# Kernel optimization log

Measured on AMD Instinct MI355X. Metric: run time of the kernel, lower is better.

The kernel has to match this reference:

```python
import jax, jax.numpy as jnp
import numpy as np

N, C, B, CTX = 1_000_000, 64, 8, 256
EPS = 1e-5


def setup_inputs() -> dict:
    key = jax.random.key(0)
    k1, k2, k3, k4, k5, k6 = jax.random.split(key, 6)
    x = jax.random.normal(k1, (N, C), dtype=jnp.float32)
    dataset_token = jax.random.normal(k2, (B, CTX), dtype=jnp.float32)
    # coors[:, 0] holds the (sorted) batch index per point; other cols are voxel coords
    batch_idx = jnp.sort(jax.random.randint(k3, (N,), 0, B))
    other = jax.random.randint(k4, (N, 3), 0, 1024)
    coors = jnp.concatenate([batch_idx[:, None], other], axis=1).astype(jnp.int64)
    # LayerNorm (base_norm) params
    gamma = jnp.ones((C,), dtype=jnp.float32)
    beta = jnp.zeros((C,), dtype=jnp.float32)
    # MLP: SiLU -> Linear(CTX, 2C)
    W = jax.random.normal(k5, (2 * C, CTX), dtype=jnp.float32) * (1.0 / np.sqrt(CTX))
    b = jax.random.normal(k6, (2 * C,), dtype=jnp.float32) * 0.02
    return {"x": x, "dataset_token": dataset_token, "gamma": gamma, "beta": beta,
            "W": W, "b": b, "coors": coors}


def reference(x, dataset_token, gamma, beta, W, b, coors):
    # base_norm = LayerNorm over features
    mu = jnp.mean(x, axis=-1, keepdims=True)
    var = jnp.mean(jnp.square(x - mu), axis=-1, keepdims=True)
    out = (x - mu) * jax.lax.rsqrt(var + EPS) * gamma + beta  # (N, C)
    # FiLM conditioning: mlp(dataset_token) -> (shift, scale) per batch element
    h = jnp.dot(jax.nn.silu(dataset_token), W.T) + b  # (B, 2C)
    shift, scale = jnp.split(h, 2, axis=1)            # each (B, C)
    idx = coors[:, 0]                                  # (N,) batch id per point
    # fused gather + affine over all N points (replaces the python loop)
    return out * (1.0 + scale[idx]) + shift[idx]
```

## Files before the change

kernel.cpp:

```cpp
#include <hip/hip_runtime.h>
#include <math.h>

#define EPS 1e-5f
#define NROWS 1000000
#define C 64
#define B 8
#define CTX 256

__global__ __launch_bounds__(1024) void token_gemm(
        const float* __restrict__ dt, const float* __restrict__ W,
        const float* __restrict__ bias, float* __restrict__ ws) {
    __shared__ float sdt[B * CTX];
    int t = threadIdx.x;
    for (int i = t; i < B * CTX; i += 1024) {
        float v = dt[i];
        sdt[i] = v / (1.0f + expf(-v));
    }
    __syncthreads();

    int j = t >> 7;
    int k = t & 127;
    const float* __restrict__ wrow = W + k * CTX;
    const float* __restrict__ drow = sdt + j * CTX;
    float acc = 0.0f;
    #pragma unroll 8
    for (int i = 0; i < CTX; ++i) acc += wrow[i] * drow[i];
    acc += bias[k];

    if (k < C) ws[j * C + k] = acc;
    else       ws[512 + j * C + (k - C)] = 1.0f + acc;
}

__global__ __launch_bounds__(256) void ln_mod(
        const float* __restrict__ x, const float* __restrict__ gamma,
        const float* __restrict__ beta, const int* __restrict__ coors,
        const float* __restrict__ h, float* __restrict__ out, int n) {
    __shared__ float sh[1024];
    int t = threadIdx.x;
    ((float4*)sh)[t] = ((const float4*)h)[t];
    __syncthreads();

    int group = t >> 4;
    int lane  = t & 15;
    int row = blockIdx.x * 16 + group;
    if (row >= n) return;

    float4 v = ((const float4*)x)[row * 16 + lane];

    float s  = v.x + v.y + v.z + v.w;
    float ss = v.x * v.x + v.y * v.y + v.z * v.z + v.w * v.w;
    #pragma unroll
    for (int m = 1; m < 16; m <<= 1) {
        s  += __shfl_xor(s,  m, 16);
        ss += __shfl_xor(ss, m, 16);
    }
    float mu   = s * (1.0f / 64.0f);
    float var  = ss * (1.0f / 64.0f) - mu * mu;
    float rstd = rsqrtf(var + EPS);

    int bidx = coors[row * 4];

    float4 g  = ((const float4*)gamma)[lane];
    float4 be = ((const float4*)beta)[lane];
    float4 sc = ((const float4*)(sh + 512 + bidx * C))[lane];
    float4 sf = ((const float4*)(sh + bidx * C))[lane];

    float4 o;
    o.x = ((v.x - mu) * rstd * g.x + be.x) * sc.x + sf.x;
    o.y = ((v.y - mu) * rstd * g.y + be.y) * sc.y + sf.y;
    o.z = ((v.z - mu) * rstd * g.z + be.z) * sc.z + sf.z;
    o.w = ((v.w - mu) * rstd * g.w + be.w) * sc.w + sf.w;

    ((float4*)out)[row * 16 + lane] = o;
}

extern "C" void kernel_launch(void* const* d_in, const int* in_sizes, int n_in,
                              void* d_out, int out_size, void* d_ws, size_t ws_size,
                              hipStream_t stream) {
    const float* x     = (const float*)d_in[0];
    const float* dt    = (const float*)d_in[1];
    const float* gamma = (const float*)d_in[2];
    const float* beta  = (const float*)d_in[3];
    const float* W     = (const float*)d_in[4];
    const float* bias  = (const float*)d_in[5];
    const int*   coors = (const int*)d_in[6];
    float* out = (float*)d_out;
    float* ws  = (float*)d_ws;

    token_gemm<<<1, 1024, 0, stream>>>(dt, W, bias, ws);

    int nblocks = (NROWS + 15) / 16;
    ln_mod<<<nblocks, 256, 0, stream>>>(x, gamma, beta, coors, ws, out, NROWS);
}
```

Measured before the change: 453.9 us.

## Parallelize token GEMM across waves and stream LN with nontemporal access

The token GEMM moves from a single 1024-thread block with serial 256-length dot products to 256 blocks in which each wave computes one output with vectorized loads and a wave shuffle reduction. The LN kernel stops staging the 4KB FiLM table in shared memory and drops its barrier, reading scale and shift directly from global memory through cache instead. The x loads and output stores become nontemporal so the streamed data does not occupy cache. This targets the serial prologue launch and the per-block barrier overhead, at the cost of more global-cache gathers per row.

```diff
diff --git a/kernel.cpp b/kernel.cpp
--- a/kernel.cpp
+++ b/kernel.cpp
@@ -7,45 +7,47 @@
 #define B 8
 #define CTX 256
 
-__global__ __launch_bounds__(1024) void token_gemm(
+typedef __attribute__((ext_vector_type(4))) float f32x4;
+
+__global__ __launch_bounds__(256) void token_gemm(
         const float* __restrict__ dt, const float* __restrict__ W,
         const float* __restrict__ bias, float* __restrict__ ws) {
-    __shared__ float sdt[B * CTX];
-    int t = threadIdx.x;
-    for (int i = t; i < B * CTX; i += 1024) {
-        float v = dt[i];
-        sdt[i] = v / (1.0f + expf(-v));
+    int wave = (blockIdx.x << 2) + (threadIdx.x >> 6);
+    int lane = threadIdx.x & 63;
+    int j = wave >> 7;
+    int k = wave & 127;
+
+    f32x4 wv = ((const f32x4*)(W  + k * CTX))[lane];
+    f32x4 dv = ((const f32x4*)(dt + j * CTX))[lane];
+
+    f32x4 s;
+    s.x = dv.x / (1.0f + expf(-dv.x));
+    s.y = dv.y / (1.0f + expf(-dv.y));
+    s.z = dv.z / (1.0f + expf(-dv.z));
+    s.w = dv.w / (1.0f + expf(-dv.w));
+
+    float acc = wv.x * s.x + wv.y * s.y + wv.z * s.z + wv.w * s.w;
+    #pragma unroll
+    for (int m = 32; m >= 1; m >>= 1) acc += __shfl_xor(acc, m, 64);
+
+    if (lane == 0) {
+        acc += bias[k];
+        if (k < C) ws[j * C + k] = acc;
+        else       ws[512 + j * C + (k - C)] = 1.0f + acc;
     }
-    __syncthreads();
-
-    int j = t >> 7;
-    int k = t & 127;
-    const float* __restrict__ wrow = W + k * CTX;
-    const float* __restrict__ drow = sdt + j * CTX;
-    float acc = 0.0f;
-    #pragma unroll 8
-    for (int i = 0; i < CTX; ++i) acc += wrow[i] * drow[i];
-    acc += bias[k];
-
-    if (k < C) ws[j * C + k] = acc;
-    else       ws[512 + j * C + (k - C)] = 1.0f + acc;
 }
 
 __global__ __launch_bounds__(256) void ln_mod(
         const float* __restrict__ x, const float* __restrict__ gamma,
         const float* __restrict__ beta, const int* __restrict__ coors,
         const float* __restrict__ h, float* __restrict__ out, int n) {
-    __shared__ float sh[1024];
     int t = threadIdx.x;
-    ((float4*)sh)[t] = ((const float4*)h)[t];
-    __syncthreads();
-
     int group = t >> 4;
     int lane  = t & 15;
     int row = blockIdx.x * 16 + group;
     if (row >= n) return;
 
-    float4 v = ((const float4*)x)[row * 16 + lane];
+    f32x4 v = __builtin_nontemporal_load((const f32x4*)x + row * 16 + lane);
 
     float s  = v.x + v.y + v.z + v.w;
     float ss = v.x * v.x + v.y * v.y + v.z * v.z + v.w * v.w;
@@ -58,20 +60,20 @@
     float var  = ss * (1.0f / 64.0f) - mu * mu;
     float rstd = rsqrtf(var + EPS);
 
-    int bidx = coors[row * 4];
+    int bidx = __ldg(coors + row * 4);
 
-    float4 g  = ((const float4*)gamma)[lane];
-    float4 be = ((const float4*)beta)[lane];
-    float4 sc = ((const float4*)(sh + 512 + bidx * C))[lane];
-    float4 sf = ((const float4*)(sh + bidx * C))[lane];
+    f32x4 g  = ((const f32x4*)gamma)[lane];
+    f32x4 be = ((const f32x4*)beta)[lane];
+    f32x4 sc = ((const f32x4*)(h + 512 + bidx * C))[lane];
+    f32x4 sf = ((const f32x4*)(h + bidx * C))[lane];
 
-    float4 o;
+    f32x4 o;
     o.x = ((v.x - mu) * rstd * g.x + be.x) * sc.x + sf.x;
     o.y = ((v.y - mu) * rstd * g.y + be.y) * sc.y + sf.y;
     o.z = ((v.z - mu) * rstd * g.z + be.z) * sc.z + sf.z;
     o.w = ((v.w - mu) * rstd * g.w + be.w) * sc.w + sf.w;
 
-    ((float4*)out)[row * 16 + lane] = o;
+    __builtin_nontemporal_store(o, (f32x4*)out + row * 16 + lane);
 }
 
 extern "C" void kernel_launch(void* const* d_in, const int* in_sizes, int n_in,
@@ -87,7 +89,7 @@
     float* out = (float*)d_out;
     float* ws  = (float*)d_ws;
 
-    token_gemm<<<1, 1024, 0, stream>>>(dt, W, bias, ws);
+    token_gemm<<<256, 256, 0, stream>>>(dt, W, bias, ws);
 
     int nblocks = (NROWS + 15) / 16;
     ln_mod<<<nblocks, 256, 0, stream>>>(x, gamma, beta, coors, ws, out, NROWS);
```

New measurement: 422.7 us. 6.9% less time.
